# Performance work log

Hardware: AMD Instinct MI355X
Metric: run time of the kernel (lower is better)

Reference implementation:

```python
import jax, jax.numpy as jnp
import numpy as np

N = 48
E = N * (N - 1)
H_LSTM = 32
EPS = 20.0

def _conv1d(x, w, b):
    # x: [B, Cin, L], w: [Cout, Cin, K] -> [B, Cout, L], 'same' padding
    y = jax.lax.conv_general_dilated(x, w, window_strides=(1,), padding='SAME',
                                     dimension_numbers=('NCH', 'OIH', 'NCH'))
    return y + b[None, :, None]

def _map(M, x):
    # map_features: linear map along dim 0 (gather for n_to_e one-hot rows,
    # incidence-sum scatter for e_to_n). M: [O, I], x: [I, ...] -> [O, ...]
    return jnp.tensordot(M, x, axes=1)

def _node_cnn(x, adj, layers, final):
    # graph conv stack: neighbor mix (adj along dim 0) + conv1d over node axis + relu
    nl = len(layers)
    for i, (w, b) in enumerate(layers):
        x = _conv1d(_map(adj, x), w, b)
        if not (final and i == nl - 1):
            x = jax.nn.relu(x)
    return x

def _node_lstm(x, mem, adj, w, b):
    # mem = cat([c, h], dim=1); gates from conv over adj-mixed cat([x, h])
    H = mem.shape[1] // 2
    c, h = mem[:, :H], mem[:, H:]
    gates = _conv1d(_map(adj, jnp.concatenate([x, h], axis=1)), w, b)
    i, f, g, o = jnp.split(gates, 4, axis=1)
    c2 = jax.nn.sigmoid(f) * c + jax.nn.sigmoid(i) * jnp.tanh(g)
    h2 = jax.nn.sigmoid(o) * jnp.tanh(c2)
    return jnp.concatenate([c2, h2], axis=1)

def _forward(bi, bij, msgi, msgj, v, nmem0, emem0, neadj, eeadj,
             e_to_n0, e_to_n1, n_to_e0, n_to_e1, decoding, params):
    fm, efm, nlstm, elstm, pp, epp = params
    n = bi.shape[0]
    e = bij.shape[0]
    # map_node_feature_to_edge
    bi_g1 = _map(n_to_e0, bi)   # [E,1,N]
    bi_g2 = _map(n_to_e1, bi)   # [E,1,N]
    # softmax (logsumexp) message computation over bij [E,1,N,N]
    cmsgi = jax.nn.logsumexp((bi_g2[:, :, None, :] + bij) * EPS, axis=3) / EPS  # [E,1,N]
    cmsgj = jax.nn.logsumexp((bi_g1[:, :, :, None] + bij) * EPS, axis=2) / EPS  # [E,1,N]
    ncmsgi = _map(e_to_n0, cmsgi)
    ncmsgj = _map(e_to_n1, cmsgj)
    nnmsgi = _map(e_to_n0, msgi)
    nnmsgj = _map(e_to_n1, msgj)
    # partial_feature (detached in original)
    dec_mat = jax.nn.one_hot(decoding, n, dtype=bi.dtype)        # [N,N]
    xi = _map(n_to_e0, dec_mat)[:, :, None]                      # [E,N,1]
    xj = _map(n_to_e1, dec_mat)[:, None, :]                      # [E,1,N]
    ep = bij.reshape(e, n, n)
    f1 = jax.lax.stop_gradient(_map(e_to_n0, (ep * xi).sum(axis=1)).reshape(n, 1, n))
    f2 = jax.lax.stop_gradient(_map(e_to_n1, (ep * xj).sum(axis=2)).reshape(n, 1, n))
    node_feature = jnp.concatenate([bi, bi + v, nnmsgi, nnmsgj, ncmsgi, ncmsgj, f1, f2], axis=1)  # [N,8,N]
    edge_feature = jnp.concatenate([msgi, msgj, cmsgi, cmsgj, bi_g1, bi_g2], axis=1)              # [E,6,N]
    nfeat = _node_cnn(node_feature, neadj, fm, False)   # [N,32,N]
    efeat = _node_cnn(edge_feature, eeadj, efm, False)  # [E,32,N]
    ntoe1, ntoe2 = _map(n_to_e0, nfeat), _map(n_to_e1, nfeat)
    eton1, eton2 = _map(e_to_n0, efeat), _map(e_to_n1, efeat)
    nfeat = jnp.concatenate([nfeat, eton1, eton2], axis=1)  # [N,96,N]
    efeat = jnp.concatenate([efeat, ntoe1, ntoe2], axis=1)  # [E,96,N]
    nmem_new = _node_lstm(nfeat, nmem0, neadj, nlstm[0], nlstm[1])  # [N,64,N]
    emem_new = _node_lstm(efeat, emem0, eeadj, elstm[0], elstm[1])  # [E,64,N]
    nfeat = nmem_new[:, H_LSTM:]   # h part
    efeat = emem_new[:, H_LSTM:]
    ntoe1, ntoe2 = _map(n_to_e0, nfeat), _map(n_to_e1, nfeat)
    eton1, eton2 = _map(e_to_n0, efeat), _map(e_to_n1, efeat)
    nfeat = jnp.concatenate([nfeat, eton1, eton2], axis=1)
    efeat = jnp.concatenate([efeat, ntoe1, ntoe2], axis=1)
    efeat = _node_cnn(efeat, eeadj, epp, True)   # [E,2,N]
    nfeat = _node_cnn(nfeat, neadj, pp, True)    # [N,1,N]
    nmsgi = efeat[:, 0:1] + 0.5 * cmsgi - msgi
    nmsgj = efeat[:, 1:2] + 0.5 * cmsgj - msgj
    nv = nfeat.mean(axis=0, keepdims=True)       # [1,1,N]
    v_out = v + nv
    bij_out = bij - nmsgi.reshape(e, 1, n, 1) - nmsgj.reshape(e, 1, 1, n)
    bi_out = bi + _map(e_to_n0, nmsgi) + _map(e_to_n1, nmsgj) - nv
    msgi_out = msgi + nmsgi
    msgj_out = msgj + nmsgj
    # get_current_dual (softmax=True)
    cdual = (v_out.sum()
             + jax.nn.logsumexp(bi_out.reshape(-1, n) * EPS, axis=1).sum() / EPS
             + jax.nn.logsumexp(bij_out.reshape(-1, n * n) * EPS, axis=1).sum() / EPS)
    return bi_out, bij_out, msgi_out, msgj_out, v_out, cdual, nmem_new, emem_new, f1, f2

def setup_inputs() -> dict:
    key = jax.random.key(0)
    ks = jax.random.split(key, 16)
    ii, jj = np.meshgrid(np.arange(N), np.arange(N), indexing='ij')
    mask = ii != jj
    src, dst = ii[mask], jj[mask]  # [E] complete directed graph
    eye = np.eye(N, dtype=np.float32)
    n_to_e0 = jnp.asarray(eye[src])  # [E,N] one-hot gather
    n_to_e1 = jnp.asarray(eye[dst])
    e_to_n0 = n_to_e0.T              # [N,E] incidence scatter-sum
    e_to_n1 = n_to_e1.T
    def glorot(k, shape):
        fan_in = shape[1] * shape[2]
        return jax.random.normal(k, shape, jnp.float32) / np.sqrt(fan_in)
    pk = jax.random.split(ks[15], 20)
    return dict(
        bi=jax.random.normal(ks[0], (N, 1, N), jnp.float32),
        bij=jax.random.normal(ks[1], (E, 1, N, N), jnp.float32),
        msgi=jnp.zeros((E, 1, N), jnp.float32),
        msgj=jnp.zeros((E, 1, N), jnp.float32),
        v=jnp.zeros((1, 1, N), jnp.float32),
        nmem0=jnp.zeros((N, 2 * H_LSTM, N), jnp.float32),
        emem0=jnp.zeros((E, 2 * H_LSTM, N), jnp.float32),
        neadj=jax.random.uniform(ks[2], (N, N), jnp.float32) / N,
        eeadj=jax.random.uniform(ks[3], (E, E), jnp.float32) / E,
        e_to_n0=e_to_n0, e_to_n1=e_to_n1, n_to_e0=n_to_e0, n_to_e1=n_to_e1,
        decoding=jax.random.randint(ks[4], (N,), 0, N),
        fm_w0=glorot(pk[0], (32, 8, 3)), fm_b0=jnp.zeros((32,), jnp.float32),
        fm_w1=glorot(pk[1], (32, 32, 3)), fm_b1=jnp.zeros((32,), jnp.float32),
        efm_w0=glorot(pk[2], (32, 6, 3)), efm_b0=jnp.zeros((32,), jnp.float32),
        efm_w1=glorot(pk[3], (32, 32, 3)), efm_b1=jnp.zeros((32,), jnp.float32),
        nlstm_w=glorot(pk[4], (128, 128, 3)), nlstm_b=jnp.zeros((128,), jnp.float32),
        elstm_w=glorot(pk[5], (128, 128, 3)), elstm_b=jnp.zeros((128,), jnp.float32),
        pp_w0=glorot(pk[6], (16, 96, 3)), pp_b0=jnp.zeros((16,), jnp.float32),
        pp_w1=glorot(pk[7], (1, 16, 3)), pp_b1=jnp.zeros((1,), jnp.float32),
        epp_w0=glorot(pk[8], (16, 96, 3)), epp_b0=jnp.zeros((16,), jnp.float32),
        epp_w1=glorot(pk[9], (2, 16, 3)), epp_b1=jnp.zeros((2,), jnp.float32),
    )

def reference(bi, bij, msgi, msgj, v, nmem0, emem0, neadj, eeadj,
              e_to_n0, e_to_n1, n_to_e0, n_to_e1, decoding,
              fm_w0, fm_b0, fm_w1, fm_b1, efm_w0, efm_b0, efm_w1, efm_b1,
              nlstm_w, nlstm_b, elstm_w, elstm_b,
              pp_w0, pp_b0, pp_w1, pp_b1, epp_w0, epp_b0, epp_w1, epp_b1):
    params = ([(fm_w0, fm_b0), (fm_w1, fm_b1)],
              [(efm_w0, efm_b0), (efm_w1, efm_b1)],
              (nlstm_w, nlstm_b), (elstm_w, elstm_b),
              [(pp_w0, pp_b0), (pp_w1, pp_b1)],
              [(epp_w0, epp_b0), (epp_w1, epp_b1)])
    return _forward(bi, bij, msgi, msgj, v, nmem0, emem0, neadj, eeadj,
                    e_to_n0, e_to_n1, n_to_e0, n_to_e1, decoding, params)
```

## Files before the change

### kernel.cpp

```cpp
#include <hip/hip_runtime.h>
#include <cstdint>
#include <cstddef>

#define EE 2256
#define EP 2304

typedef __attribute__((ext_vector_type(8))) short bf16x8;
typedef __attribute__((ext_vector_type(4))) float f32x4;

__device__ __forceinline__ unsigned short f2b(float f){
  unsigned u = __builtin_bit_cast(unsigned, f);
  u += 0x7fffu + ((u>>16)&1u);
  return (unsigned short)(u>>16);
}
__device__ __forceinline__ float b2f(unsigned short h){
  unsigned u = ((unsigned)h)<<16; return __builtin_bit_cast(float, u);
}
__device__ __forceinline__ float sigm(float x){ return 1.f/(1.f+__expf(-x)); }
__device__ __forceinline__ float tanhfast(float x){ return 1.f - 2.f/(__expf(2.f*x)+1.f); }

__device__ __forceinline__ int xcd_swz(int bid, int nwg){
  int xcd = bid & 7, idx = bid >> 3;
  int q = nwg >> 3, r = nwg & 7;
  return (xcd < r ? xcd*(q+1) : r*(q+1) + (xcd-r)*q) + idx;
}

typedef __attribute__((address_space(3))) unsigned int lds_u32;
typedef __attribute__((address_space(1))) const unsigned int gbl_u32;
__device__ __forceinline__ void glds16(const void* g, void* l){
  __builtin_amdgcn_global_load_lds((gbl_u32*)g, (lds_u32*)l, 16, 0, 0);
}

__global__ __launch_bounds__(128) void gm_zero_pads(unsigned short* yp6, unsigned short* yp32,
                                                    unsigned short* yp128, unsigned short* yp16){
  int e = blockIdx.x; int tid = threadIdx.x;
  #pragma unroll
  for (int r=0; r<2; ++r){
    int row = r ? 49 : 0;
    if (tid < 8)  yp6 [((size_t)e*50+row)*8  + tid] = 0;
    if (tid < 32) yp32[((size_t)e*50+row)*32 + tid] = 0;
    yp128[((size_t)e*50+row)*128 + tid] = 0;
    if (tid < 16) yp16[((size_t)e*50+row)*16 + tid] = 0;
  }
}

__global__ void gm_prep_eeadj(const float* __restrict__ src, unsigned short* __restrict__ dst){
  int idx = blockIdx.x*256 + threadIdx.x;
  if (idx >= EP*EP) return;
  int r = idx / EP, k = idx - r*EP;
  float v = (r < EE && k < EE) ? src[(size_t)r*EE + k] : 0.f;
  dst[idx] = f2b(v);
}

__global__ void gm_prep_wall(const float* __restrict__ w0, const float* __restrict__ w1,
                             const float* __restrict__ w2, const float* __restrict__ w3,
                             const float* __restrict__ w4,
                             unsigned short* d0, unsigned short* d1, unsigned short* d2,
                             unsigned short* d3, unsigned short* d4){
  int idx = blockIdx.x*256 + threadIdx.x;
  const float* w; unsigned short* dp; int Co,Cin,KPT,Kpad,loc;
  if      (idx < 1024) { w=w0; dp=d0; Co=32;  Cin=6;   KPT=8;   Kpad=32;  loc=idx; }
  else if (idx < 4096) { w=w1; dp=d1; Co=32;  Cin=32;  KPT=32;  Kpad=96;  loc=idx-1024; }
  else if (idx < 53248){ w=w2; dp=d2; Co=128; Cin=128; KPT=128; Kpad=384; loc=idx-4096; }
  else if (idx < 57856){ w=w3; dp=d3; Co=16;  Cin=96;  KPT=96;  Kpad=288; loc=idx-53248; }
  else if (idx < 58880){ w=w4; dp=d4; Co=2;   Cin=16;  KPT=16;  Kpad=64;  loc=idx-57856; }
  else return;
  int co = loc / Kpad; int k = loc - co*Kpad;
  int t = k / KPT; int ci = k - t*KPT;
  float v = (co < Co && t < 3 && ci < Cin) ? w[((size_t)co*Cin + ci)*3 + t] : 0.f;
  dp[loc] = f2b(v);
}

__global__ __launch_bounds__(128) void gm_cmsg(const float* __restrict__ bi, const float* __restrict__ bij,
                                               float* __restrict__ cmi, float* __restrict__ cmj){
  int e = blockIdx.x; int tid = threadIdx.x;
  __shared__ float t[48*49]; __shared__ float bs[48], bd[48];
  const float* src = bij + (size_t)e*2304;
  for (int i=tid;i<2304;i+=128){ int r=i/48, c=i-r*48; t[r*49+c]=src[i]; }
  if (tid<48){ int s=e/47, m=e-s*47; int d=m+(m>=s); bs[tid]=bi[s*48+tid]; bd[tid]=bi[d*48+tid]; }
  __syncthreads();
  if (tid < 48){
    float mx=-1e30f;
    for (int n=0;n<48;n++) mx = fmaxf(mx, t[tid*49+n]+bd[n]);
    float sm=0.f;
    for (int n=0;n<48;n++) sm += __expf((t[tid*49+n]+bd[n]-mx)*20.f);
    cmi[e*48+tid] = mx + __logf(sm)*(1.f/20.f);
  } else if (tid>=64 && tid<112){
    int n = tid-64;
    float mx=-1e30f;
    for (int k=0;k<48;k++) mx = fmaxf(mx, t[k*49+n]+bs[k]);
    float sm=0.f;
    for (int k=0;k<48;k++) sm += __expf((t[k*49+n]+bs[k]-mx)*20.f);
    cmj[e*48+n] = mx + __logf(sm)*(1.f/20.f);
  }
}

__global__ __launch_bounds__(256) void gm_node_accum(const float* __restrict__ bij, const float* __restrict__ cmi,
                              const float* __restrict__ cmj, const float* __restrict__ msgi,
                              const float* __restrict__ msgj, const int* __restrict__ dec,
                              float* ncmi, float* ncmj, float* nnmi, float* nnmj,
                              float* o_f1, float* o_f2){
  int i = blockIdx.x; int tid = threadIdx.x;
  __shared__ float red[5][6][48];
  int mg = tid / 48;
  int w  = tid - mg*48;
  if (mg < 5){
    int dc = dec[i];
    float a1=0,a2=0,a3=0,a4=0,s1=0,s2=0;
    for (int m=mg; m<47; m+=5){
      int e1 = i*47+m;
      a1 += cmi[e1*48+w]; a3 += msgi[e1*48+w];
      s1 += bij[(size_t)e1*2304 + dc*48 + w];
      int j = m + (m>=i); int e2 = j*47 + i - (i>j);
      a2 += cmj[e2*48+w]; a4 += msgj[e2*48+w];
      s2 += bij[(size_t)e2*2304 + w*48 + dc];
    }
    red[mg][0][w]=a1; red[mg][1][w]=a2; red[mg][2][w]=a3;
    red[mg][3][w]=a4; red[mg][4][w]=s1; red[mg][5][w]=s2;
  }
  __syncthreads();
  if (tid < 48){
    float a1=0,a2=0,a3=0,a4=0,s1=0,s2=0;
    for (int g=0; g<5; g++){
      a1+=red[g][0][tid]; a2+=red[g][1][tid]; a3+=red[g][2][tid];
      a4+=red[g][3][tid]; s1+=red[g][4][tid]; s2+=red[g][5][tid];
    }
    ncmi[i*48+tid]=a1; ncmj[i*48+tid]=a2; nnmi[i*48+tid]=a3; nnmj[i*48+tid]=a4;
    o_f1[i*48+tid]=s1; o_f2[i*48+tid]=s2;
  }
}

__global__ void gm_build_x6(const float* __restrict__ msgi, const float* __restrict__ msgj,
                            const float* __restrict__ cmi, const float* __restrict__ cmj,
                            const float* __restrict__ bi, unsigned short* __restrict__ x6){
  int idx = blockIdx.x*256 + threadIdx.x;
  if (idx >= 6*EP) return;
  int c = idx / EP, e = idx - c*EP;
  if (e >= EE){ for (int w=0;w<48;w++) x6[(size_t)(w*6+c)*EP + e] = 0; return; }
  int s = e/47, m = e-s*47, d = m + (m>=s);
  for (int w=0; w<48; w++){
    float x;
    switch(c){
      case 0: x = msgi[e*48+w]; break;
      case 1: x = msgj[e*48+w]; break;
      case 2: x = cmi[e*48+w]; break;
      case 3: x = cmj[e*48+w]; break;
      case 4: x = bi[s*48+w]; break;
      default: x = bi[d*48+w]; break;
    }
    x6[(size_t)(w*6+c)*EP + e] = f2b(x);
  }
}

__global__ void gm_fill_x128_hi(const float* __restrict__ emem0, const float* __restrict__ nfeat,
                                unsigned short* __restrict__ x128){
  int idx = blockIdx.x*256 + threadIdx.x;
  if (idx >= 96*EP) return;
  int q = idx/EP; int c = 32 + q; int e = idx - q*EP;
  if (e >= EE){ for (int w=0;w<48;w++) x128[(size_t)(w*128+c)*EP + e] = 0; return; }
  int s=e/47, m=e-s*47, d=m+(m>=s);
  const float* srcrow;
  if (c < 64)      srcrow = nfeat + ((size_t)s*32 + (c-32))*48;
  else if (c < 96) srcrow = nfeat + ((size_t)d*32 + (c-64))*48;
  else             srcrow = emem0 + ((size_t)e*64 + (c-64))*48;
  #pragma unroll
  for (int w4=0; w4<12; w4++){
    float4 xv = *(const float4*)(srcrow + w4*4);
    x128[(size_t)((w4*4+0)*128+c)*EP + e] = f2b(xv.x);
    x128[(size_t)((w4*4+1)*128+c)*EP + e] = f2b(xv.y);
    x128[(size_t)((w4*4+2)*128+c)*EP + e] = f2b(xv.z);
    x128[(size_t)((w4*4+3)*128+c)*EP + e] = f2b(xv.w);
  }
}

__global__ __launch_bounds__(256) void gm_map_gemm(
    const unsigned short* __restrict__ A, const unsigned short* __restrict__ BT,
    unsigned short* __restrict__ ypad, float* __restrict__ outf,
    const float* __restrict__ bias, int ncol, int Nvalid, int Cch, int Cslab, int do_relu, int f32_out)
{
  __shared__ __align__(16) unsigned short lA[128*32];
  __shared__ __align__(16) unsigned short lB[128*32];
  const int tid = threadIdx.x;
  const int lane = tid & 63, wid = tid >> 6;
  const int swz = xcd_swz(blockIdx.x, gridDim.x);
  const int m0 = (swz / ncol) * 128;
  const int n0 = (swz % ncol) * 128;
  const int wm = wid >> 1, wn = wid & 1;
  f32x4 acc[4][4];
  #pragma unroll
  for (int i=0;i<4;i++){
    #pragma unroll
    for (int j=0;j<4;j++) acc[i][j] = f32x4{0.f,0.f,0.f,0.f};
  }
  const int srow = (lane>>2), scol = (lane&3);

  for (int ks = 0; ks < EP/32; ++ks) {
    #pragma unroll
    for (int q=0;q<2;q++){
      int chunk = wid*2+q;
      int row = chunk*16 + srow;
      int off = (scol*16) ^ (((row>>1)&3)<<4);
      glds16((const char*)A  + (size_t)(m0+row)*(EP*2) + ks*64 + off, (char*)lA + chunk*1024);
      glds16((const char*)BT + (size_t)(n0+row)*(EP*2) + ks*64 + off, (char*)lB + chunk*1024);
    }
    __syncthreads();
    bf16x8 af[4], bfr[4];
    #pragma unroll
    for (int mi=0;mi<4;mi++){
      int row = wm*64 + mi*16 + (lane&15);
      int off = ((lane>>4)*16) ^ (((row>>1)&3)<<4);
      af[mi] = *(const bf16x8*)((const char*)lA + row*64 + off);
    }
    #pragma unroll
    for (int ni=0;ni<4;ni++){
      int row = wn*64 + ni*16 + (lane&15);
      int off = ((lane>>4)*16) ^ (((row>>1)&3)<<4);
      bfr[ni] = *(const bf16x8*)((const char*)lB + row*64 + off);
    }
    #pragma unroll
    for (int mi=0;mi<4;mi++){
      #pragma unroll
      for (int ni=0;ni<4;ni++)
        acc[mi][ni] = __builtin_amdgcn_mfma_f32_16x16x32_bf16(af[mi], bfr[ni], acc[mi][ni], 0,0,0);
    }
    __syncthreads();
  }
  #pragma unroll
  for (int mi=0;mi<4;mi++){
    int ebase = m0 + wm*64 + mi*16 + (lane>>4)*4;
    #pragma unroll
    for (int ni=0;ni<4;ni++){
      int c = n0 + wn*64 + ni*16 + (lane&15);
      if (c >= Nvalid) continue;
      int w = c / Cch, ci = c - w*Cch;
      float bv = bias ? bias[ci] : 0.f;
      #pragma unroll
      for (int r=0;r<4;r++){
        int e = ebase + r;
        if (e >= EE) continue;
        float x = acc[mi][ni][r] + bv;
        if (do_relu) x = fmaxf(x, 0.f);
        if (f32_out) outf[(size_t)e*Nvalid + c] = x;
        else ypad[((size_t)e*50 + 1 + w)*Cslab + ci] = f2b(x);
      }
    }
  }
}

template<int BM>
__global__ __launch_bounds__(256) void gm_conv_gemm(
    const unsigned short* __restrict__ Wp, const unsigned short* __restrict__ ypad,
    unsigned short* __restrict__ outT, const float* __restrict__ bias,
    int Cch, int KPT, int Kpad, int Co, int Ct, int do_relu)
{
  constexpr int MI = (BM==128)?4:((BM==32)?2:1);
  constexpr int NI = (BM==128)?4:2;
  __shared__ __align__(16) unsigned short lA[BM*32];
  __shared__ __align__(16) unsigned short lB[128*32];
  const int tid = threadIdx.x, lane = tid&63, wid = tid>>6;
  const int swz = xcd_swz(blockIdx.x, 864);
  const int e0 = (swz / 48) * 128;
  const int w  = swz % 48;
  const int rowb = (BM==128)? (wid>>1)*64 : 0;
  const int colb = (BM==128)? (wid&1)*64 : wid*32;
  f32x4 acc[MI][NI];
  #pragma unroll
  for (int i=0;i<MI;i++){
    #pragma unroll
    for (int j=0;j<NI;j++) acc[i][j] = f32x4{0.f,0.f,0.f,0.f};
  }
  const int srow=(lane>>2), scol=(lane&3);
  const int ksteps = Kpad/32;
  for (int ks=0; ks<ksteps; ++ks){
    for (int c = wid; c < BM/16; c += 4){
      int row = c*16 + srow;
      int off = (scol*16) ^ (((row>>1)&3)<<4);
      glds16((const char*)Wp + (size_t)row*(Kpad*2) + ks*64 + off, (char*)lA + c*1024);
    }
    for (int c = wid; c < 8; c += 4){
      int row = c*16 + srow;
      int off = (scol*16) ^ (((row>>1)&3)<<4);
      int kg = ks*32 + (off>>1);
      int t = kg / KPT;
      int ci = kg - t*KPT;
      int e = e0 + row;
      const char* src;
      if (t < 3 && e < EE) src = (const char*)ypad + ((size_t)(e*50 + w + t)*Cch + ci)*2;
      else                 src = (const char*)ypad;
      glds16(src, (char*)lB + c*1024);
    }
    __syncthreads();
    bf16x8 af[MI], bfr[NI];
    #pragma unroll
    for (int mi=0;mi<MI;mi++){
      int row = rowb + mi*16 + (lane&15);
      int off = ((lane>>4)*16) ^ (((row>>1)&3)<<4);
      af[mi] = *(const bf16x8*)((const char*)lA + row*64 + off);
    }
    #pragma unroll
    for (int ni=0;ni<NI;ni++){
      int row = colb + ni*16 + (lane&15);
      int off = ((lane>>4)*16) ^ (((row>>1)&3)<<4);
      bfr[ni] = *(const bf16x8*)((const char*)lB + row*64 + off);
    }
    #pragma unroll
    for (int mi=0;mi<MI;mi++){
      #pragma unroll
      for (int ni=0;ni<NI;ni++)
        acc[mi][ni] = __builtin_amdgcn_mfma_f32_16x16x32_bf16(af[mi], bfr[ni], acc[mi][ni], 0,0,0);
    }
    __syncthreads();
  }
  #pragma unroll
  for (int mi=0;mi<MI;mi++){
    #pragma unroll
    for (int ni=0;ni<NI;ni++){
      int m = colb + ni*16 + (lane&15);
      int e = e0 + m;
      if (e >= EE) continue;
      #pragma unroll
      for (int r=0;r<4;r++){
        int co = rowb + mi*16 + (lane>>4)*4 + r;
        if (co >= Co) continue;
        float x = acc[mi][ni][r] + (bias ? bias[co] : 0.f);
        if (do_relu) x = fmaxf(x, 0.f);
        outT[((size_t)(w*Ct + co))*EP + e] = f2b(x);
      }
    }
  }
}

__global__ void gm_build_nf(const float* __restrict__ bi, const float* __restrict__ v,
                            const float* __restrict__ nnmi, const float* __restrict__ nnmj,
                            const float* __restrict__ ncmi, const float* __restrict__ ncmj,
                            const float* __restrict__ f1, const float* __restrict__ f2,
                            float* __restrict__ nf){
  int idx = blockIdx.x*256+threadIdx.x;
  if (idx >= 48*8*48) return;
  int i = idx/(8*48); int rem = idx - i*(8*48); int c = rem/48; int w = rem-c*48;
  int iw = i*48+w;
  float x;
  switch(c){
    case 0: x=bi[iw]; break;
    case 1: x=bi[iw]+v[w]; break;
    case 2: x=nnmi[iw]; break;
    case 3: x=nnmj[iw]; break;
    case 4: x=ncmi[iw]; break;
    case 5: x=ncmj[iw]; break;
    case 6: x=f1[iw]; break;
    default: x=f2[iw]; break;
  }
  nf[idx]=x;
}

__global__ void gm_nmap(const float* __restrict__ adj, const float* __restrict__ X,
                        float* __restrict__ Y, int C){
  int idx = blockIdx.x*256 + threadIdx.x;
  int tot = 48*C*48;
  if (idx >= tot) return;
  int i = idx/(C*48); int rem = idx - i*(C*48);
  float s=0.f;
  for (int j=0;j<48;j++) s += adj[i*48+j]*X[(size_t)j*C*48 + rem];
  Y[idx]=s;
}

__global__ void gm_nconv(const float* __restrict__ X, const float* __restrict__ wgt,
                         const float* __restrict__ bias, float* __restrict__ Y,
                         int Cin, int Co, int relu){
  int idx = blockIdx.x*256 + threadIdx.x;
  int tot = 48*Co*48;
  if (idx >= tot) return;
  int i = idx/(Co*48); int rem = idx - i*(Co*48); int co = rem/48; int w = rem-co*48;
  float s = bias[co];
  const float* xb = X + (size_t)i*Cin*48;
  const float* wb = wgt + (size_t)co*Cin*3;
  for (int ci=0; ci<Cin; ++ci){
    float w0 = wb[ci*3], w1 = wb[ci*3+1], w2 = wb[ci*3+2];
    const float* xr = xb + ci*48;
    if (w > 0) s += xr[w-1]*w0;
    s += xr[w]*w1;
    if (w < 47) s += xr[w+1]*w2;
  }
  if (relu) s = fmaxf(s, 0.f);
  Y[idx] = s;
}

__global__ __launch_bounds__(256) void gm_nconv_lstm(const float* __restrict__ X,
    const float* __restrict__ wgt, const float* __restrict__ bias,
    const float* __restrict__ nmem0, float* __restrict__ o_nmem, float* __restrict__ nfeat2){
  int idx = blockIdx.x*256 + threadIdx.x;
  if (idx >= 48*32*48) return;
  int i = idx/(32*48); int rem = idx - i*(32*48); int ch = rem/48; int w = rem-ch*48;
  const float* xb = X + (size_t)i*128*48;
  float s0=bias[ch], s1=bias[32+ch], s2=bias[64+ch], s3=bias[96+ch];
  for (int ci=0; ci<128; ++ci){
    const float* xr = xb + ci*48;
    float xm = (w>0)? xr[w-1] : 0.f;
    float xc = xr[w];
    float xp = (w<47)? xr[w+1] : 0.f;
    const float* wb0 = wgt + ((size_t)ch*128+ci)*3;
    const float* wb1 = wgt + ((size_t)(32+ch)*128+ci)*3;
    const float* wb2 = wgt + ((size_t)(64+ch)*128+ci)*3;
    const float* wb3 = wgt + ((size_t)(96+ch)*128+ci)*3;
    s0 += xm*wb0[0]+xc*wb0[1]+xp*wb0[2];
    s1 += xm*wb1[0]+xc*wb1[1]+xp*wb1[2];
    s2 += xm*wb2[0]+xc*wb2[1]+xp*wb2[2];
    s3 += xm*wb3[0]+xc*wb3[1]+xp*wb3[2];
  }
  float c = nmem0[((size_t)i*64+ch)*48+w];
  float c2 = sigm(s1)*c + sigm(s0)*tanhfast(s2);
  float h2 = sigm(s3)*tanhfast(c2);
  o_nmem[((size_t)i*64+ch)*48+w] = c2;
  o_nmem[((size_t)i*64+32+ch)*48+w] = h2;
  nfeat2[((size_t)i*32+ch)*48+w] = h2;
}

__global__ __launch_bounds__(256) void gm_eton_x128(const unsigned short* __restrict__ x128,
                                                    float* __restrict__ xn){
  int row = blockIdx.x;
  int w = row >> 5, cc = row & 31;
  __shared__ float L[2256];
  const unsigned short* src = x128 + (size_t)(w*128 + cc)*EP;
  for (int t=threadIdx.x; t<2256; t+=256) L[t] = b2f(src[t]);
  __syncthreads();
  int tid = threadIdx.x;
  if (tid < 48){
    int i = tid; float s=0.f;
    for (int m=0;m<47;m++) s += L[i*47+m];
    xn[((size_t)i*128 + 32 + cc)*48 + w] = s;
  } else if (tid >= 64 && tid < 112){
    int i = tid-64; float s=0.f;
    for (int m=0;m<47;m++){
      int j = m + (m>=i);
      s += L[j*47 + i - (i>j)];
    }
    xn[((size_t)i*128 + 64 + cc)*48 + w] = s;
  }
}

__global__ void gm_xnode_copy(const float* __restrict__ nfeat, const float* __restrict__ nmem0,
                              float* __restrict__ xn){
  int idx = blockIdx.x*256+threadIdx.x;
  if (idx >= 48*64*48) return;
  int i = idx/(64*48); int rem = idx - i*(64*48); int c = rem/48; int w = rem-c*48;
  if (c < 32) xn[((size_t)i*128 + c)*48 + w] = nfeat[((size_t)i*32+c)*48+w];
  else        xn[((size_t)i*128 + 96 + (c-32))*48 + w] = nmem0[((size_t)i*64 + 32 + (c-32))*48 + w];
}

__global__ __launch_bounds__(256) void gm_elstm_pw(const unsigned short* __restrict__ gatesT,
                                                   const float* __restrict__ emem0,
                                                   float* __restrict__ o_emem){
  int bid = blockIdx.x;
  int e4 = bid / 6, chunk = bid - e4*6;
  int cw = chunk*256 + threadIdx.x;
  int ch = cw / 48, w = cw - ch*48;
  int ebase = e4*4;
  const unsigned short* g0 = gatesT + (size_t)(w*128 + ch)*EP + ebase;
  ushort4 vi = *(const ushort4*)(g0);
  ushort4 vf = *(const ushort4*)(g0 + (size_t)32*EP);
  ushort4 vg = *(const ushort4*)(g0 + (size_t)64*EP);
  ushort4 vo = *(const ushort4*)(g0 + (size_t)96*EP);
  const unsigned short* pi = (const unsigned short*)&vi;
  const unsigned short* pf = (const unsigned short*)&vf;
  const unsigned short* pg = (const unsigned short*)&vg;
// ... 17 lines not shown
  for (int t=threadIdx.x; t<2256; t+=256)
    L[t] = o_emem[((size_t)t*64 + 32 + cc)*48 + w];
  __syncthreads();
  int tid = threadIdx.x;
  if (tid < 48){
    int i=tid; float s=0.f;
    for (int m=0;m<47;m++) s += L[i*47+m];
    x2[((size_t)i*96 + 32 + cc)*48 + w] = s;
  } else if (tid>=64 && tid<112){
    int i=tid-64; float s=0.f;
    for (int m=0;m<47;m++){ int j=m+(m>=i); s += L[j*47 + i - (i>j)]; }
    x2[((size_t)i*96 + 64 + cc)*48 + w] = s;
  }
}

__global__ void gm_x2_copy(const float* __restrict__ nfeat2, float* __restrict__ x2){
  int idx = blockIdx.x*256+threadIdx.x;
  if (idx >= 48*32*48) return;
  int i = idx/(32*48); int rem = idx - i*(32*48); int c = rem/48; int w = rem-c*48;
  x2[((size_t)i*96 + c)*48 + w] = nfeat2[idx];
}

__global__ __launch_bounds__(128) void gm_build_xpp(const float* __restrict__ o_emem,
                                                    const float* __restrict__ nfeat2,
                                                    unsigned short* __restrict__ xpp){
  int e = blockIdx.x; int tid = threadIdx.x;
  __shared__ float h[1536];
  __shared__ float sn[3072];
  int s = e/47; int m = e - s*47; int d = m + (m>=s);
  const float* src = o_emem + ((size_t)e*64 + 32)*48;
  for (int i=tid;i<1536;i+=128) h[i]=src[i];
  const float* ps = nfeat2 + (size_t)s*32*48;
  const float* pd = nfeat2 + (size_t)d*32*48;
  for (int i=tid;i<1536;i+=128){ sn[i]=ps[i]; sn[1536+i]=pd[i]; }
  if (tid < 96){
    xpp[((size_t)e*50 + 0)*96 + tid] = 0;
    xpp[((size_t)e*50 + 49)*96 + tid] = 0;
  }
  __syncthreads();
  for (int w=0; w<48; w++){
    if (tid < 96){
      float x;
      if (tid<32) x = h[tid*48+w];
      else x = sn[(tid-32)*48 + w];
      xpp[((size_t)e*50 + 1 + w)*96 + tid] = f2b(x);
    }
  }
}

__global__ void gm_nv(const float* __restrict__ nfpp, const float* __restrict__ v,
                      float* __restrict__ nv, float* __restrict__ o_v){
  int w = threadIdx.x;
  if (w<48){
    float s=0.f; for (int i=0;i<48;i++) s += nfpp[i*48+w];
    s *= (1.f/48.f);
    nv[w]=s; o_v[w]=v[w]+s;
  }
}

__global__ __launch_bounds__(256) void gm_bijout(const float* __restrict__ bij,
                                                 const float* __restrict__ effpp,
                                                 const float* __restrict__ cmi, const float* __restrict__ cmj,
                                                 const float* __restrict__ msgi, const float* __restrict__ msgj,
                                                 float* __restrict__ nmi, float* __restrict__ nmj,
                                                 float* __restrict__ o_mi, float* __restrict__ o_mj,
                                                 float* __restrict__ o_bij, float* __restrict__ lse_e){
  int e = blockIdx.x; int tid = threadIdx.x;
  __shared__ float ri[48], rj[48], red[8];
  if (tid < 48){
    int idx = e*48+tid;
    float a = effpp[(size_t)e*96 + tid*2] + 0.5f*cmi[idx] - msgi[idx];
    ri[tid] = a; nmi[idx] = a; o_mi[idx] = msgi[idx] + a;
  } else if (tid >= 64 && tid < 112){
    int t2 = tid-64; int idx = e*48+t2;
    float b = effpp[(size_t)e*96 + t2*2 + 1] + 0.5f*cmj[idx] - msgj[idx];
    rj[t2] = b; nmj[idx] = b; o_mj[idx] = msgj[idx] + b;
  }
  __syncthreads();
  float v[9]; float mx = -1e30f;
  const float* src = bij + (size_t)e*2304;
  float* dst = o_bij + (size_t)e*2304;
  #pragma unroll
  for (int q=0;q<9;q++){
    int idx = q*256 + tid;
    int r = idx/48, c = idx-r*48;
    float x = src[idx] - ri[r] - rj[c];
    dst[idx] = x; v[q] = x; mx = fmaxf(mx, x);
  }
  for (int o=1;o<64;o<<=1) mx = fmaxf(mx, __shfl_xor(mx, o, 64));
  int lane = tid&63, w4 = tid>>6;
  if (lane==0) red[w4] = mx;
  __syncthreads();
  mx = fmaxf(fmaxf(red[0],red[1]),fmaxf(red[2],red[3]));
  float s = 0.f;
  #pragma unroll
  for (int q=0;q<9;q++) s += __expf((v[q]-mx)*20.f);
  for (int o=1;o<64;o<<=1) s += __shfl_xor(s, o, 64);
  if (lane==0) red[4+w4] = s;
  __syncthreads();
  if (tid==0){
    float t = red[4]+red[5]+red[6]+red[7];
    lse_e[e] = mx + __logf(t)*(1.f/20.f);
  }
}

__global__ void gm_biout(const float* __restrict__ bi, const float* __restrict__ nmi,
                         const float* __restrict__ nmj, const float* __restrict__ nv,
                         float* __restrict__ o_bi, float* __restrict__ lse_n){
  int i = blockIdx.x; int w = threadIdx.x;
  float val = -1e30f;
  if (w < 48){
    float s = 0.f;
    for (int m=0;m<47;m++){
      int e1 = i*47+m;
      s += nmi[e1*48+w];
      int j = m + (m>=i);
      int e2 = j*47 + i - (i>j);
      s += nmj[e2*48+w];
    }
    val = bi[i*48+w] + s - nv[w];
    o_bi[i*48+w] = val;
  }
  float mx = val;
  for (int o=1;o<64;o<<=1) mx = fmaxf(mx, __shfl_xor(mx, o, 64));
  float ex = (w<48)? __expf((val-mx)*20.f) : 0.f;
  for (int o=1;o<64;o<<=1) ex += __shfl_xor(ex, o, 64);
  if (w==0) lse_n[i] = mx + __logf(ex)*(1.f/20.f);
}

__global__ void gm_cdual(const float* __restrict__ lse_e, const float* __restrict__ lse_n,
                         const float* __restrict__ vout, float* __restrict__ out){
  int tid = threadIdx.x;
  float s = 0.f;
  for (int i=tid;i<EE;i+=256) s += lse_e[i];
  if (tid<48) s += lse_n[tid] + vout[tid];
  __shared__ float red[4];
  for (int o=1;o<64;o<<=1) s += __shfl_xor(s,o,64);
  if ((tid&63)==0) red[tid>>6]=s;
  __syncthreads();
  if (tid==0) out[0] = red[0]+red[1]+red[2]+red[3];
}

static constexpr size_t A256v(size_t x){ return (x+255)&~(size_t)255; }
static constexpr size_t OFF_EEADJ = 0;
static constexpr size_t OFF_X6T   = A256v(OFF_EEADJ + (size_t)EP*EP*2);
static constexpr size_t OFF_X32T  = A256v(OFF_X6T  + (size_t)384*EP*2);
static constexpr size_t OFF_X128T = A256v(OFF_X32T + (size_t)1536*EP*2);
static constexpr size_t OFF_YP6   = A256v(OFF_X128T + (size_t)6144*EP*2);
static constexpr size_t OFF_YP32  = A256v(OFF_YP6  + (size_t)EE*50*8*2);
static constexpr size_t OFF_YP128 = A256v(OFF_YP32 + (size_t)EE*50*32*2);
static constexpr size_t OFF_YP16  = A256v(OFF_YP128 + (size_t)EE*50*128*2);
static constexpr size_t OFF_ZEND  = A256v(OFF_YP16 + (size_t)EE*50*16*2 + 256);
static constexpr size_t OFF_XPP   = OFF_YP128;
static constexpr size_t OFF_WC0 = OFF_ZEND;
static constexpr size_t OFF_WC1 = A256v(OFF_WC0 + 32*32*2);
static constexpr size_t OFF_WCL = A256v(OFF_WC1 + 32*96*2);
static constexpr size_t OFF_WP0 = A256v(OFF_WCL + 128*384*2);
static constexpr size_t OFF_WP1 = A256v(OFF_WP0 + 16*288*2);
static constexpr size_t OFF_CMI = A256v(OFF_WP1 + 16*64*2);
static constexpr size_t OFF_CMJ = A256v(OFF_CMI + (size_t)EE*48*4);
static constexpr size_t OFF_NMI = A256v(OFF_CMJ + (size_t)EE*48*4);
static constexpr size_t OFF_NMJ = A256v(OFF_NMI + (size_t)EE*48*4);
static constexpr size_t OFF_EFPP= A256v(OFF_NMJ + (size_t)EE*48*4);
static constexpr size_t OFF_LSEE= A256v(OFF_EFPP + (size_t)EE*96*4);
static constexpr size_t OFF_LSEN= A256v(OFF_LSEE + EE*4);
static constexpr size_t OFF_NV  = A256v(OFF_LSEN + 48*4);
static constexpr size_t OFF_NF  = A256v(OFF_NV + 48*4);
static constexpr size_t OFF_NT1 = A256v(OFF_NF + (size_t)48*8*48*4);
static constexpr size_t OFF_NT2 = A256v(OFF_NT1 + (size_t)48*128*48*4);
static constexpr size_t OFF_NFEAT = A256v(OFF_NT2 + (size_t)48*128*48*4);
static constexpr size_t OFF_NFEAT2= A256v(OFF_NFEAT + (size_t)48*32*48*4);
static constexpr size_t OFF_XN  = A256v(OFF_NFEAT2 + (size_t)48*32*48*4);
static constexpr size_t OFF_NFPP= A256v(OFF_XN + (size_t)48*128*48*4);
static constexpr size_t OFF_NAC = A256v(OFF_NFPP + (size_t)48*48*4);

extern "C" void kernel_launch(void* const* d_in, const int* in_sizes, int n_in,
                              void* d_out, int out_size, void* d_ws, size_t ws_size,
                              hipStream_t stream) {
  const float* bi    = (const float*)d_in[0];
  const float* bij   = (const float*)d_in[1];
  const float* msgi  = (const float*)d_in[2];
  const float* msgj  = (const float*)d_in[3];
  const float* v_in  = (const float*)d_in[4];
  const float* nmem0 = (const float*)d_in[5];
  const float* emem0 = (const float*)d_in[6];
  const float* neadj = (const float*)d_in[7];
  const float* eeadj = (const float*)d_in[8];
  const int*   dec   = (const int*)d_in[13];
  const float* fm_w0 = (const float*)d_in[14]; const float* fm_b0 = (const float*)d_in[15];
  const float* fm_w1 = (const float*)d_in[16]; const float* fm_b1 = (const float*)d_in[17];
  const float* efm_w0= (const float*)d_in[18]; const float* efm_b0= (const float*)d_in[19];
  const float* efm_w1= (const float*)d_in[20]; const float* efm_b1= (const float*)d_in[21];
  const float* nl_w  = (const float*)d_in[22]; const float* nl_b  = (const float*)d_in[23];
  const float* el_w  = (const float*)d_in[24]; const float* el_b  = (const float*)d_in[25];
  const float* pp_w0 = (const float*)d_in[26]; const float* pp_b0 = (const float*)d_in[27];
  const float* pp_w1 = (const float*)d_in[28]; const float* pp_b1 = (const float*)d_in[29];
  const float* epp_w0= (const float*)d_in[30]; const float* epp_b0= (const float*)d_in[31];
  const float* epp_w1= (const float*)d_in[32]; const float* epp_b1= (const float*)d_in[33];

  char* ws = (char*)d_ws;
  unsigned short* eeadjb = (unsigned short*)(ws + OFF_EEADJ);
  unsigned short* x6t    = (unsigned short*)(ws + OFF_X6T);
  unsigned short* x32t   = (unsigned short*)(ws + OFF_X32T);
  unsigned short* x128t  = (unsigned short*)(ws + OFF_X128T);
  unsigned short* z1t    = x32t;
  unsigned short* z2t    = x6t;
  unsigned short* gatesT = x128t;
  unsigned short* yp6    = (unsigned short*)(ws + OFF_YP6);
  unsigned short* yp32   = (unsigned short*)(ws + OFF_YP32);
  unsigned short* yp128  = (unsigned short*)(ws + OFF_YP128);
  unsigned short* yp16   = (unsigned short*)(ws + OFF_YP16);
  unsigned short* xpp    = (unsigned short*)(ws + OFF_XPP);
  unsigned short* wc0 = (unsigned short*)(ws + OFF_WC0);
  unsigned short* wc1 = (unsigned short*)(ws + OFF_WC1);
  unsigned short* wcl = (unsigned short*)(ws + OFF_WCL);
  unsigned short* wp0 = (unsigned short*)(ws + OFF_WP0);
  unsigned short* wp1 = (unsigned short*)(ws + OFF_WP1);
  float* cmi  = (float*)(ws + OFF_CMI);
  float* cmj  = (float*)(ws + OFF_CMJ);
  float* nmi  = (float*)(ws + OFF_NMI);
  float* nmj  = (float*)(ws + OFF_NMJ);
  float* effpp= (float*)(ws + OFF_EFPP);
  float* lse_e= (float*)(ws + OFF_LSEE);
  float* lse_n= (float*)(ws + OFF_LSEN);
  float* nvb  = (float*)(ws + OFF_NV);
  float* nf   = (float*)(ws + OFF_NF);
  float* nt1  = (float*)(ws + OFF_NT1);
  float* nt2  = (float*)(ws + OFF_NT2);
  float* nfeat  = (float*)(ws + OFF_NFEAT);
  float* nfeat2 = (float*)(ws + OFF_NFEAT2);
  float* xn   = (float*)(ws + OFF_XN);
  float* nfpp = (float*)(ws + OFF_NFPP);
  float* ncmi = (float*)(ws + OFF_NAC);
  float* ncmj = ncmi + 2304;
  float* nnmi = ncmi + 2*2304;
  float* nnmj = ncmi + 3*2304;

  float* out = (float*)d_out;
  float* o_bi   = out;
  float* o_bij  = out + 2304;
  float* o_mi   = out + 2304 + 5197824;
  float* o_mj   = o_mi + 108288;
  float* o_v    = o_mj + 108288;
  float* o_cd   = o_v + 48;
  float* o_nmem = o_cd + 1;
  float* o_emem = o_nmem + 147456;
  float* o_f1   = o_emem + 6930432;
  float* o_f2   = o_f1 + 2304;

  gm_zero_pads<<<EE, 128, 0, stream>>>(yp6, yp32, yp128, yp16);
  gm_prep_eeadj<<<(EP*EP+255)/256, 256, 0, stream>>>(eeadj, eeadjb);
  gm_prep_wall<<<(58880+255)/256, 256, 0, stream>>>(efm_w0, efm_w1, el_w, epp_w0, epp_w1,
                                                    wc0, wc1, wcl, wp0, wp1);
  gm_cmsg<<<EE, 128, 0, stream>>>(bi, bij, cmi, cmj);
  gm_node_accum<<<48, 256, 0, stream>>>(bij, cmi, cmj, msgi, msgj, dec, ncmi, ncmj, nnmi, nnmj, o_f1, o_f2);
  gm_build_x6<<<(6*EP+255)/256, 256, 0, stream>>>(msgi, msgj, cmi, cmj, bi, x6t);
  gm_build_nf<<<(48*8*48+255)/256, 256, 0, stream>>>(bi, v_in, nnmi, nnmj, ncmi, ncmj, o_f1, o_f2, nf);
  gm_nmap<<<(48*8*48+255)/256, 256, 0, stream>>>(neadj, nf, nt1, 8);
  gm_nconv<<<(48*32*48+255)/256, 256, 0, stream>>>(nt1, fm_w0, fm_b0, nt2, 8, 32, 1);
  gm_nmap<<<(48*32*48+255)/256, 256, 0, stream>>>(neadj, nt2, nt1, 32);
  gm_nconv<<<(48*32*48+255)/256, 256, 0, stream>>>(nt1, fm_w1, fm_b1, nfeat, 32, 32, 1);
  gm_map_gemm<<<54,  256, 0, stream>>>(eeadjb, x6t,  yp6,  nullptr, nullptr, 3, 288, 6, 8, 0, 0);
  gm_conv_gemm<32><<<864, 256, 0, stream>>>(wc0, yp6,  x32t, efm_b0, 8, 8, 32, 32, 32, 1);
  gm_map_gemm<<<216, 256, 0, stream>>>(eeadjb, x32t, yp32, nullptr, nullptr, 12, 1536, 32, 32, 0, 0);
  gm_conv_gemm<32><<<864, 256, 0, stream>>>(wc1, yp32, x128t, efm_b1, 32, 32, 96, 32, 128, 1);
  gm_fill_x128_hi<<<(96*EP+255)/256, 256, 0, stream>>>(emem0, nfeat, x128t);
  gm_xnode_copy<<<(48*64*48+255)/256, 256, 0, stream>>>(nfeat, nmem0, xn);
  gm_eton_x128<<<1536, 256, 0, stream>>>(x128t, xn);
  gm_nmap<<<(48*128*48+255)/256, 256, 0, stream>>>(neadj, xn, nt1, 128);
  gm_nconv_lstm<<<(48*32*48+255)/256, 256, 0, stream>>>(nt1, nl_w, nl_b, nmem0, o_nmem, nfeat2);
  gm_map_gemm<<<864, 256, 0, stream>>>(eeadjb, x128t, yp128, nullptr, nullptr, 48, 6144, 128, 128, 0, 0);
  gm_conv_gemm<128><<<864, 256, 0, stream>>>(wcl, yp128, gatesT, el_b, 128, 128, 384, 128, 128, 0);
  gm_elstm_pw<<<564*6, 256, 0, stream>>>(gatesT, emem0, o_emem);
  gm_build_xpp<<<EE, 128, 0, stream>>>(o_emem, nfeat2, xpp);
  gm_conv_gemm<16><<<864, 256, 0, stream>>>(wp0, xpp,  z1t, nullptr, 96, 96, 288, 16, 16, 0);
  gm_map_gemm<<<108, 256, 0, stream>>>(eeadjb, z1t, yp16, nullptr, epp_b0, 6, 768, 16, 16, 1, 0);
  gm_conv_gemm<16><<<864, 256, 0, stream>>>(wp1, yp16, z2t, nullptr, 16, 16, 64, 2, 2, 0);
  gm_map_gemm<<<18, 256, 0, stream>>>(eeadjb, z2t, nullptr, effpp, epp_b1, 1, 96, 2, 2, 0, 1);
  gm_x2_copy<<<(48*32*48+255)/256, 256, 0, stream>>>(nfeat2, xn);
  gm_eton_h<<<1536, 256, 0, stream>>>(o_emem, xn);
  gm_nmap<<<(48*96*48+255)/256, 256, 0, stream>>>(neadj, xn, nt1, 96);
  gm_nconv<<<(48*16*48+255)/256, 256, 0, stream>>>(nt1, pp_w0, pp_b0, nt2, 96, 16, 1);
  gm_nmap<<<(48*16*48+255)/256, 256, 0, stream>>>(neadj, nt2, nt1, 16);
  gm_nconv<<<(48*1*48+255)/256, 256, 0, stream>>>(nt1, pp_w1, pp_b1, nfpp, 16, 1, 0);
  gm_nv<<<1, 64, 0, stream>>>(nfpp, v_in, nvb, o_v);
  gm_bijout<<<EE, 256, 0, stream>>>(bij, effpp, cmi, cmj, msgi, msgj, nmi, nmj, o_mi, o_mj, o_bij, lse_e);
  gm_biout<<<48, 64, 0, stream>>>(bi, nmi, nmj, nvb, o_bi, lse_n);
  gm_cdual<<<1, 256, 0, stream>>>(lse_e, lse_n, o_v, o_cd);
}
```

Before: 876.7 us.

## Add split-K map GEMM, double-buffer LDS staging, and coalesce x6 build

Introduces a split-K variant of the edge-adjacency GEMM, writing partial sums to a float workspace with a separate reduction kernel, and uses it for the low-column GEMMs (6, 16 and 2 channel) that launched too few workgroups to fill the device. The LDS staging in both the map and conv GEMMs becomes double-buffered so the next K-slice loads while MFMAs run on the current one. The tile order switches to row-major-in-M. The x6 build kernel is parallelised per output element for coalesced writes. The split-K workspace aliases the yp128 buffer, so that buffer's pad zeroing moves to just before its use. The cost is extra kernel launches, partial-sum memory traffic and doubled LDS use.

New measurement: 811.7 us. 1.08x faster.

```diff
diff --git a/kernel.cpp b/kernel.cpp
--- a/kernel.cpp
+++ b/kernel.cpp
@@ -32,16 +32,21 @@
 }
 
 __global__ __launch_bounds__(128) void gm_zero_pads(unsigned short* yp6, unsigned short* yp32,
-                                                    unsigned short* yp128, unsigned short* yp16){
+                                                    unsigned short* yp16){
   int e = blockIdx.x; int tid = threadIdx.x;
   #pragma unroll
   for (int r=0; r<2; ++r){
     int row = r ? 49 : 0;
     if (tid < 8)  yp6 [((size_t)e*50+row)*8  + tid] = 0;
     if (tid < 32) yp32[((size_t)e*50+row)*32 + tid] = 0;
-    yp128[((size_t)e*50+row)*128 + tid] = 0;
     if (tid < 16) yp16[((size_t)e*50+row)*16 + tid] = 0;
   }
+}
+
+__global__ __launch_bounds__(128) void gm_zero_pad128(unsigned short* yp128){
+  int e = blockIdx.x; int tid = threadIdx.x;
+  yp128[((size_t)e*50+0)*128 + tid] = 0;
+  yp128[((size_t)e*50+49)*128 + tid] = 0;
 }
 
 __global__ void gm_prep_eeadj(const float* __restrict__ src, unsigned short* __restrict__ dst){
@@ -134,11 +139,12 @@
                             const float* __restrict__ cmi, const float* __restrict__ cmj,
                             const float* __restrict__ bi, unsigned short* __restrict__ x6){
   int idx = blockIdx.x*256 + threadIdx.x;
-  if (idx >= 6*EP) return;
-  int c = idx / EP, e = idx - c*EP;
-  if (e >= EE){ for (int w=0;w<48;w++) x6[(size_t)(w*6+c)*EP + e] = 0; return; }
-  int s = e/47, m = e-s*47, d = m + (m>=s);
-  for (int w=0; w<48; w++){
+  if (idx >= 288*EP) return;
+  int row = idx / EP, e = idx - row*EP;
+  int w = row / 6, c = row - w*6;
+  unsigned short val = 0;
+  if (e < EE){
+    int s = e/47, m = e-s*47, d = m + (m>=s);
     float x;
     switch(c){
       case 0: x = msgi[e*48+w]; break;
@@ -148,8 +154,9 @@
       case 4: x = bi[s*48+w]; break;
       default: x = bi[d*48+w]; break;
     }
-    x6[(size_t)(w*6+c)*EP + e] = f2b(x);
-  }
+    val = f2b(x);
+  }
+  x6[idx] = val;
 }
 
 __global__ void gm_fill_x128_hi(const float* __restrict__ emem0, const float* __restrict__ nfeat,
@@ -176,15 +183,16 @@
 __global__ __launch_bounds__(256) void gm_map_gemm(
     const unsigned short* __restrict__ A, const unsigned short* __restrict__ BT,
     unsigned short* __restrict__ ypad, float* __restrict__ outf,
-    const float* __restrict__ bias, int ncol, int Nvalid, int Cch, int Cslab, int do_relu, int f32_out)
+    const float* __restrict__ bias, int nrow, int Nvalid, int Cch, int Cslab,
+    int do_relu, int f32_out)
 {
-  __shared__ __align__(16) unsigned short lA[128*32];
-  __shared__ __align__(16) unsigned short lB[128*32];
+  __shared__ __align__(16) unsigned short lA[2][128*32];
+  __shared__ __align__(16) unsigned short lB[2][128*32];
   const int tid = threadIdx.x;
   const int lane = tid & 63, wid = tid >> 6;
   const int swz = xcd_swz(blockIdx.x, gridDim.x);
-  const int m0 = (swz / ncol) * 128;
-  const int n0 = (swz % ncol) * 128;
+  const int m0 = (swz % nrow) * 128;
+  const int n0 = (swz / nrow) * 128;
   const int wm = wid >> 1, wn = wid & 1;
   f32x4 acc[4][4];
   #pragma unroll
@@ -194,28 +202,29 @@
   }
   const int srow = (lane>>2), scol = (lane&3);
 
-  for (int ks = 0; ks < EP/32; ++ks) {
+  auto STAGE = [&](int ks, int b){
     #pragma unroll
     for (int q=0;q<2;q++){
       int chunk = wid*2+q;
       int row = chunk*16 + srow;
       int off = (scol*16) ^ (((row>>1)&3)<<4);
-      glds16((const char*)A  + (size_t)(m0+row)*(EP*2) + ks*64 + off, (char*)lA + chunk*1024);
-      glds16((const char*)BT + (size_t)(n0+row)*(EP*2) + ks*64 + off, (char*)lB + chunk*1024);
-    }
-    __syncthreads();
+      glds16((const char*)A  + (size_t)(m0+row)*(EP*2) + ks*64 + off, (char*)lA[b] + chunk*1024);
+      glds16((const char*)BT + (size_t)(n0+row)*(EP*2) + ks*64 + off, (char*)lB[b] + chunk*1024);
+    }
+  };
+  auto COMPUTE = [&](int b){
     bf16x8 af[4], bfr[4];
     #pragma unroll
     for (int mi=0;mi<4;mi++){
       int row = wm*64 + mi*16 + (lane&15);
       int off = ((lane>>4)*16) ^ (((row>>1)&3)<<4);
-      af[mi] = *(const bf16x8*)((const char*)lA + row*64 + off);
+      af[mi] = *(const bf16x8*)((const char*)lA[b] + row*64 + off);
     }
     #pragma unroll
     for (int ni=0;ni<4;ni++){
       int row = wn*64 + ni*16 + (lane&15);
       int off = ((lane>>4)*16) ^ (((row>>1)&3)<<4);
-      bfr[ni] = *(const bf16x8*)((const char*)lB + row*64 + off);
+      bfr[ni] = *(const bf16x8*)((const char*)lB[b] + row*64 + off);
     }
     #pragma unroll
     for (int mi=0;mi<4;mi++){
@@ -223,7 +232,16 @@
       for (int ni=0;ni<4;ni++)
         acc[mi][ni] = __builtin_amdgcn_mfma_f32_16x16x32_bf16(af[mi], bfr[ni], acc[mi][ni], 0,0,0);
     }
+  };
+
+  STAGE(0, 0);
+  __syncthreads();
+  int cur = 0;
+  for (int ks = 0; ks < EP/32; ++ks){
+    if (ks+1 < EP/32) STAGE(ks+1, cur^1);
+    COMPUTE(cur);
     __syncthreads();
+    cur ^= 1;
   }
   #pragma unroll
   for (int mi=0;mi<4;mi++){
@@ -247,6 +265,101 @@
   }
 }
 
+__global__ __launch_bounds__(256) void gm_map_sk(
+    const unsigned short* __restrict__ A, const unsigned short* __restrict__ BT,
+    float* __restrict__ pbuf, int nrow, int ncol, int S, int kspan)
+{
+  __shared__ __align__(16) unsigned short lA[2][128*32];
+  __shared__ __align__(16) unsigned short lB[2][128*32];
+  const int tid = threadIdx.x;
+  const int lane = tid & 63, wid = tid >> 6;
+  const int swz = xcd_swz(blockIdx.x, gridDim.x);
+  const int ntile = nrow*ncol;
+  const int sp = swz / ntile;
+  const int tile = swz - sp*ntile;
+  const int m0 = (tile % nrow) * 128;
+  const int n0 = (tile / nrow) * 128;
+  const int Npad = ncol*128;
+  const int k0 = sp*kspan, k1 = k0 + kspan;
+  const int wm = wid >> 1, wn = wid & 1;
+  f32x4 acc[4][4];
+  #pragma unroll
+  for (int i=0;i<4;i++){
+    #pragma unroll
+    for (int j=0;j<4;j++) acc[i][j] = f32x4{0.f,0.f,0.f,0.f};
+  }
+  const int srow = (lane>>2), scol = (lane&3);
+
+  auto STAGE = [&](int ks, int b){
+    #pragma unroll
+    for (int q=0;q<2;q++){
+      int chunk = wid*2+q;
+      int row = chunk*16 + srow;
+      int off = (scol*16) ^ (((row>>1)&3)<<4);
+      glds16((const char*)A  + (size_t)(m0+row)*(EP*2) + ks*64 + off, (char*)lA[b] + chunk*1024);
+      glds16((const char*)BT + (size_t)(n0+row)*(EP*2) + ks*64 + off, (char*)lB[b] + chunk*1024);
+    }
+  };
+  auto COMPUTE = [&](int b){
+    bf16x8 af[4], bfr[4];
+    #pragma unroll
+    for (int mi=0;mi<4;mi++){
+      int row = wm*64 + mi*16 + (lane&15);
+      int off = ((lane>>4)*16) ^ (((row>>1)&3)<<4);
+      af[mi] = *(const bf16x8*)((const char*)lA[b] + row*64 + off);
+    }
+    #pragma unroll
+    for (int ni=0;ni<4;ni++){
+      int row = wn*64 + ni*16 + (lane&15);
+      int off = ((lane>>4)*16) ^ (((row>>1)&3)<<4);
+      bfr[ni] = *(const bf16x8*)((const char*)lB[b] + row*64 + off);
+    }
+    #pragma unroll
+    for (int mi=0;mi<4;mi++){
+      #pragma unroll
+      for (int ni=0;ni<4;ni++)
+        acc[mi][ni] = __builtin_amdgcn_mfma_f32_16x16x32_bf16(af[mi], bfr[ni], acc[mi][ni], 0,0,0);
+    }
+  };
+
+  STAGE(k0, 0);
+  __syncthreads();
+  int cur = 0;
+  for (int ks = k0; ks < k1; ++ks){
+    if (ks+1 < k1) STAGE(ks+1, cur^1);
+    COMPUTE(cur);
+    __syncthreads();
+    cur ^= 1;
+  }
+  float* pb = pbuf + (size_t)sp*2304*Npad;
+  #pragma unroll
+  for (int mi=0;mi<4;mi++){
+    int ebase = m0 + wm*64 + mi*16 + (lane>>4)*4;
+    #pragma unroll
+    for (int ni=0;ni<4;ni++){
+      int c = n0 + wn*64 + ni*16 + (lane&15);
+      #pragma unroll
+      for (int r=0;r<4;r++)
+        pb[(size_t)(ebase+r)*Npad + c] = acc[mi][ni][r];
+    }
+  }
+}
+
+__global__ void gm_sk_fin(const float* __restrict__ pbuf, unsigned short* __restrict__ ypad,
+                          float* __restrict__ outf, const float* __restrict__ bias,
+                          int S, int Npad, int Nvalid, int Cch, int Cslab, int do_relu, int f32_out){
+  int idx = blockIdx.x*256 + threadIdx.x;
+  if (idx >= EE*Nvalid) return;
+  int e = idx / Nvalid, c = idx - e*Nvalid;
+  float s = 0.f;
+  for (int p=0;p<S;p++) s += pbuf[(size_t)p*2304*Npad + (size_t)e*Npad + c];
+  int w = c / Cch, ci = c - w*Cch;
+  if (bias) s += bias[ci];
+  if (do_relu) s = fmaxf(s, 0.f);
+  if (f32_out) outf[(size_t)e*Nvalid + c] = s;
+  else ypad[((size_t)e*50 + 1 + w)*Cslab + ci] = f2b(s);
+}
+
 template<int BM>
 __global__ __launch_bounds__(256) void gm_conv_gemm(
     const unsigned short* __restrict__ Wp, const unsigned short* __restrict__ ypad,
@@ -255,8 +368,8 @@
 {
   constexpr int MI = (BM==128)?4:((BM==32)?2:1);
   constexpr int NI = (BM==128)?4:2;
-  __shared__ __align__(16) unsigned short lA[BM*32];
-  __shared__ __align__(16) unsigned short lB[128*32];
+  __shared__ __align__(16) unsigned short lA[2][BM*32];
+  __shared__ __align__(16) unsigned short lB[2][128*32];
   const int tid = threadIdx.x, lane = tid&63, wid = tid>>6;
   const int swz = xcd_swz(blockIdx.x, 864);
   const int e0 = (swz / 48) * 128;
@@ -271,11 +384,12 @@
   }
   const int srow=(lane>>2), scol=(lane&3);
   const int ksteps = Kpad/32;
-  for (int ks=0; ks<ksteps; ++ks){
+
+  auto STAGE = [&](int ks, int b){
     for (int c = wid; c < BM/16; c += 4){
       int row = c*16 + srow;
       int off = (scol*16) ^ (((row>>1)&3)<<4);
-      glds16((const char*)Wp + (size_t)row*(Kpad*2) + ks*64 + off, (char*)lA + c*1024);
+      glds16((const char*)Wp + (size_t)row*(Kpad*2) + ks*64 + off, (char*)lA[b] + c*1024);
     }
     for (int c = wid; c < 8; c += 4){
       int row = c*16 + srow;
@@ -287,21 +401,22 @@
       const char* src;
       if (t < 3 && e < EE) src = (const char*)ypad + ((size_t)(e*50 + w + t)*Cch + ci)*2;
       else                 src = (const char*)ypad;
-      glds16(src, (char*)lB + c*1024);
-    }
-    __syncthreads();
+      glds16(src, (char*)lB[b] + c*1024);
+    }
+  };
+  auto COMPUTE = [&](int b){
     bf16x8 af[MI], bfr[NI];
     #pragma unroll
     for (int mi=0;mi<MI;mi++){
       int row = rowb + mi*16 + (lane&15);
       int off = ((lane>>4)*16) ^ (((row>>1)&3)<<4);
-      af[mi] = *(const bf16x8*)((const char*)lA + row*64 + off);
+      af[mi] = *(const bf16x8*)((const char*)lA[b] + row*64 + off);
     }
     #pragma unroll
     for (int ni=0;ni<NI;ni++){
       int row = colb + ni*16 + (lane&15);
       int off = ((lane>>4)*16) ^ (((row>>1)&3)<<4);
-      bfr[ni] = *(const bf16x8*)((const char*)lB + row*64 + off);
+      bfr[ni] = *(const bf16x8*)((const char*)lB[b] + row*64 + off);
     }
     #pragma unroll
     for (int mi=0;mi<MI;mi++){
@@ -309,7 +424,16 @@
       for (int ni=0;ni<NI;ni++)
         acc[mi][ni] = __builtin_amdgcn_mfma_f32_16x16x32_bf16(af[mi], bfr[ni], acc[mi][ni], 0,0,0);
     }
+  };
+
+  STAGE(0, 0);
+  __syncthreads();
+  int cur = 0;
+  for (int ks=0; ks<ksteps; ++ks){
+    if (ks+1 < ksteps) STAGE(ks+1, cur^1);
+    COMPUTE(cur);
     __syncthreads();
+    cur ^= 1;
   }
   #pragma unroll
   for (int mi=0;mi<MI;mi++){
@@ -633,6 +757,7 @@
 static constexpr size_t OFF_YP16  = A256v(OFF_YP128 + (size_t)EE*50*128*2);
 static constexpr size_t OFF_ZEND  = A256v(OFF_YP16 + (size_t)EE*50*16*2 + 256);
 static constexpr size_t OFF_XPP   = OFF_YP128;
+static constexpr size_t OFF_SKP   = OFF_YP128;
 static constexpr size_t OFF_WC0 = OFF_ZEND;
 static constexpr size_t OFF_WC1 = A256v(OFF_WC0 + 32*32*2);
 static constexpr size_t OFF_WCL = A256v(OFF_WC1 + 32*96*2);
@@ -692,6 +817,7 @@
   unsigned short* yp128  = (unsigned short*)(ws + OFF_YP128);
   unsigned short* yp16   = (unsigned short*)(ws + OFF_YP16);
   unsigned short* xpp    = (unsigned short*)(ws + OFF_XPP);
+  float*          skp    = (float*)(ws + OFF_SKP);
   unsigned short* wc0 = (unsigned short*)(ws + OFF_WC0);
   unsigned short* wc1 = (unsigned short*)(ws + OFF_WC1);
   unsigned short* wcl = (unsigned short*)(ws + OFF_WCL);
@@ -729,35 +855,39 @@
   float* o_f1   = o_emem + 6930432;
   float* o_f2   = o_f1 + 2304;
 
-  gm_zero_pads<<<EE, 128, 0, stream>>>(yp6, yp32, yp128, yp16);
+  gm_zero_pads<<<EE, 128, 0, stream>>>(yp6, yp32, yp16);
   gm_prep_eeadj<<<(EP*EP+255)/256, 256, 0, stream>>>(eeadj, eeadjb);
   gm_prep_wall<<<(58880+255)/256, 256, 0, stream>>>(efm_w0, efm_w1, el_w, epp_w0, epp_w1,
                                                     wc0, wc1, wcl, wp0, wp1);
   gm_cmsg<<<EE, 128, 0, stream>>>(bi, bij, cmi, cmj);
   gm_node_accum<<<48, 256, 0, stream>>>(bij, cmi, cmj, msgi, msgj, dec, ncmi, ncmj, nnmi, nnmj, o_f1, o_f2);
-  gm_build_x6<<<(6*EP+255)/256, 256, 0, stream>>>(msgi, msgj, cmi, cmj, bi, x6t);
+  gm_build_x6<<<(288*EP+255)/256, 256, 0, stream>>>(msgi, msgj, cmi, cmj, bi, x6t);
   gm_build_nf<<<(48*8*48+255)/256, 256, 0, stream>>>(bi, v_in, nnmi, nnmj, ncmi, ncmj, o_f1, o_f2, nf);
   gm_nmap<<<(48*8*48+255)/256, 256, 0, stream>>>(neadj, nf, nt1, 8);
   gm_nconv<<<(48*32*48+255)/256, 256, 0, stream>>>(nt1, fm_w0, fm_b0, nt2, 8, 32, 1);
   gm_nmap<<<(48*32*48+255)/256, 256, 0, stream>>>(neadj, nt2, nt1, 32);
   gm_nconv<<<(48*32*48+255)/256, 256, 0, stream>>>(nt1, fm_w1, fm_b1, nfeat, 32, 32, 1);
-  gm_map_gemm<<<54,  256, 0, stream>>>(eeadjb, x6t,  yp6,  nullptr, nullptr, 3, 288, 6, 8, 0, 0);
+  gm_map_sk<<<216, 256, 0, stream>>>(eeadjb, x6t, skp, 18, 3, 4, 18);
+  gm_sk_fin<<<(EE*288+255)/256, 256, 0, stream>>>(skp, yp6, nullptr, nullptr, 4, 384, 288, 6, 8, 0, 0);
   gm_conv_gemm<32><<<864, 256, 0, stream>>>(wc0, yp6,  x32t, efm_b0, 8, 8, 32, 32, 32, 1);
-  gm_map_gemm<<<216, 256, 0, stream>>>(eeadjb, x32t, yp32, nullptr, nullptr, 12, 1536, 32, 32, 0, 0);
+  gm_map_gemm<<<216, 256, 0, stream>>>(eeadjb, x32t, yp32, nullptr, nullptr, 18, 1536, 32, 32, 0, 0);
   gm_conv_gemm<32><<<864, 256, 0, stream>>>(wc1, yp32, x128t, efm_b1, 32, 32, 96, 32, 128, 1);
   gm_fill_x128_hi<<<(96*EP+255)/256, 256, 0, stream>>>(emem0, nfeat, x128t);
   gm_xnode_copy<<<(48*64*48+255)/256, 256, 0, stream>>>(nfeat, nmem0, xn);
   gm_eton_x128<<<1536, 256, 0, stream>>>(x128t, xn);
   gm_nmap<<<(48*128*48+255)/256, 256, 0, stream>>>(neadj, xn, nt1, 128);
   gm_nconv_lstm<<<(48*32*48+255)/256, 256, 0, stream>>>(nt1, nl_w, nl_b, nmem0, o_nmem, nfeat2);
-  gm_map_gemm<<<864, 256, 0, stream>>>(eeadjb, x128t, yp128, nullptr, nullptr, 48, 6144, 128, 128, 0, 0);
+  gm_zero_pad128<<<EE, 128, 0, stream>>>(yp128);
+  gm_map_gemm<<<864, 256, 0, stream>>>(eeadjb, x128t, yp128, nullptr, nullptr, 18, 6144, 128, 128, 0, 0);
   gm_conv_gemm<128><<<864, 256, 0, stream>>>(wcl, yp128, gatesT, el_b, 128, 128, 384, 128, 128, 0);
   gm_elstm_pw<<<564*6, 256, 0, stream>>>(gatesT, emem0, o_emem);
   gm_build_xpp<<<EE, 128, 0, stream>>>(o_emem, nfeat2, xpp);
   gm_conv_gemm<16><<<864, 256, 0, stream>>>(wp0, xpp,  z1t, nullptr, 96, 96, 288, 16, 16, 0);
-  gm_map_gemm<<<108, 256, 0, stream>>>(eeadjb, z1t, yp16, nullptr, epp_b0, 6, 768, 16, 16, 1, 0);
+  gm_map_sk<<<432, 256, 0, stream>>>(eeadjb, z1t, skp, 18, 6, 4, 18);
+  gm_sk_fin<<<(EE*768+255)/256, 256, 0, stream>>>(skp, yp16, nullptr, epp_b0, 4, 768, 768, 16, 16, 1, 0);
   gm_conv_gemm<16><<<864, 256, 0, stream>>>(wp1, yp16, z2t, nullptr, 16, 16, 64, 2, 2, 0);
-  gm_map_gemm<<<18, 256, 0, stream>>>(eeadjb, z2t, nullptr, effpp, epp_b1, 1, 96, 2, 2, 0, 1);
+  gm_map_sk<<<144, 256, 0, stream>>>(eeadjb, z2t, skp, 18, 1, 8, 9);
+  gm_sk_fin<<<(EE*96+255)/256, 256, 0, stream>>>(skp, nullptr, effpp, epp_b1, 8, 128, 96, 2, 2, 0, 1);
   gm_x2_copy<<<(48*32*48+255)/256, 256, 0, stream>>>(nfeat2, xn);
   gm_eton_h<<<1536, 256, 0, stream>>>(o_emem, xn);
   gm_nmap<<<(48*96*48+255)/256, 256, 0, stream>>>(neadj, xn, nt1, 96);
```
